# Performance work log

Measured on AMD Instinct MI355X. Metric: run time of the kernel, lower is better.

The kernel has to match this reference:

```python
import jax, jax.numpy as jnp
import numpy as np

N, E = 50000, 800000
D, H, EDIM, DFF = 128, 8, 16, 512
C = D // H  # per-head channels
NEG_SLOPE_GAT = 0.2
NEG_SLOPE = 0.01
EPS_LN = 1e-6


def layer_norm(x, g, b):
    mu = x.mean(-1, keepdims=True)
    sd = x.std(-1, keepdims=True, ddof=1)  # torch std default (unbiased)
    return g * (x - mu) / (sd + EPS_LN) + b


def gat_conv(x, ei, ew, W, a_src, a_dst, We, a_e, bias):
    # PyG GATConv with edge_dim, concat=True, eval mode (no dropout)
    n = x.shape[0]
    xh = (x @ W).reshape(n, H, C)            # [N,H,C]
    s_src = (xh * a_src).sum(-1)             # [N,H]
    s_dst = (xh * a_dst).sum(-1)             # [N,H]
    eh = (ew @ We).reshape(-1, H, C)         # [E,H,C]
    s_e = (eh * a_e).sum(-1)                 # [E,H]
    src, dst = ei[0], ei[1]
    alpha = jax.nn.leaky_relu(s_src[src] + s_dst[dst] + s_e, NEG_SLOPE_GAT)  # [E,H]
    # segment softmax over destination nodes
    m = jax.ops.segment_max(alpha, dst, num_segments=n)
    alpha = jnp.exp(alpha - m[dst])
    z = jax.ops.segment_sum(alpha, dst, num_segments=n)
    alpha = alpha / (z[dst] + 1e-16)
    msg = xh[src] * alpha[..., None]         # [E,H,C]
    out = jax.ops.segment_sum(msg, dst, num_segments=n)  # [N,H,C]
    return out.reshape(n, H * C) + bias


def setup_inputs() -> dict:
    key = jax.random.key(0)
    ks = jax.random.split(key, 32)
    p = lambda k, sh: (jax.random.normal(k, sh, dtype=jnp.float32) * 0.02)
    inp = {
        "nf": jax.random.normal(ks[0], (N, D), dtype=jnp.float32),
        "ei": jax.random.randint(ks[1], (2, E), 0, N, dtype=jnp.int32),
        "ew": jax.random.normal(ks[2], (E, EDIM), dtype=jnp.float32),
        # GATConv 1
        "W1": p(ks[3], (D, H * C)), "as1": p(ks[4], (H, C)), "ad1": p(ks[5], (H, C)),
        "We1": p(ks[6], (EDIM, H * C)), "ae1": p(ks[7], (H, C)), "b1": jnp.zeros((H * C,), jnp.float32),
        "g1": jnp.ones((D,), jnp.float32), "be1": jnp.zeros((D,), jnp.float32),
        # GATConv 2
        "W2": p(ks[8], (D, H * C)), "as2": p(ks[9], (H, C)), "ad2": p(ks[10], (H, C)),
        "We2": p(ks[11], (EDIM, H * C)), "ae2": p(ks[12], (H, C)), "b2": jnp.zeros((H * C,), jnp.float32),
        "g2": jnp.ones((D,), jnp.float32), "be2": jnp.zeros((D,), jnp.float32),
        # FFN + norm3
        "Wf1": p(ks[13], (D, DFF)), "bf1": jnp.zeros((DFF,), jnp.float32),
        "Wf2": p(ks[14], (DFF, D)), "bf2": jnp.zeros((D,), jnp.float32),
        "g3": jnp.ones((D,), jnp.float32), "be3": jnp.zeros((D,), jnp.float32),
    }
    return inp


def reference(nf, ei, ew, W1, as1, ad1, We1, ae1, b1, g1, be1,
              W2, as2, ad2, We2, ae2, b2, g2, be2,
              Wf1, bf1, Wf2, bf2, g3, be3):
    # gnn_mode == 'res', eval mode (dropout = identity)
    h = gat_conv(nf, ei, ew, W1, as1, ad1, We1, ae1, b1)
    nf = nf + jax.nn.leaky_relu(layer_norm(h, g1, be1), NEG_SLOPE)
    h = gat_conv(nf, ei, ew, W2, as2, ad2, We2, ae2, b2)
    nf = nf + jax.nn.leaky_relu(layer_norm(h, g2, be2), NEG_SLOPE)
    ff = jax.nn.relu(nf @ Wf1 + bf1) @ Wf2 + bf2
    nf = nf + jax.nn.leaky_relu(layer_norm(ff, g3, be3), NEG_SLOPE)
    return nf
```

## Files before the change

kernel.cpp:

```cpp
#include <hip/hip_runtime.h>
#include <hip/hip_bf16.h>

#define NN 50000
#define NE 800000
#define DD 128
#define HH 8
#define CC 16
#define DFF 512
#define ED 16
#define SCAN_NB ((NN + 255) / 256)
#define BKT 256
#define NBKT ((NN + BKT - 1) / BKT)
#define EPB 4096

typedef __attribute__((ext_vector_type(8))) short bf16x8;
typedef __attribute__((ext_vector_type(4))) float f32x4;

union U8 { bf16x8 v; unsigned short s[8]; };

__device__ inline unsigned short f2bf(float f) {
    union { float f; unsigned u; } v; v.f = f;
    return (unsigned short)((v.u + 0x7fffu + ((v.u >> 16) & 1u)) >> 16);
}
__device__ inline float bf2f(unsigned s) {
    union { unsigned u; float f; } v; v.u = s << 16;
    return v.f;
}

__global__ void zero_int_k(int* __restrict__ a, int n) {
    int i = blockIdx.x * 256 + threadIdx.x;
    if (i < n) a[i] = 0;
}

__global__ void cvtpack_k(const float* __restrict__ W, unsigned short* __restrict__ Wpk,
                          int K, int N) {
    int idx = blockIdx.x * 256 + threadIdx.x;
    if (idx >= K * N) return;
    int e = idx & 7;
    int l = (idx >> 3) & 63;
    int r = idx >> 9;
    int n16 = N >> 4;
    int jc = r % n16;
    int kt = r / n16;
    int k = kt * 32 + (l >> 4) * 8 + e;
    int n = jc * 16 + (l & 15);
    Wpk[idx] = f2bf(W[(size_t)k * N + n]);
}

__global__ void count_k(const int* __restrict__ dst, int* __restrict__ cnt) {
    int e = blockIdx.x * 256 + threadIdx.x;
    if (e < NE) atomicAdd(&cnt[dst[e]], 1);
}

__global__ void blksum_k(const int* __restrict__ cnt, int* __restrict__ partials) {
    int i = blockIdx.x * 256 + threadIdx.x;
    int v = (i < NN) ? cnt[i] : 0;
#pragma unroll
    for (int m = 1; m < 64; m <<= 1) v += __shfl_xor(v, m, 64);
    __shared__ int ws[4];
    if ((threadIdx.x & 63) == 0) ws[threadIdx.x >> 6] = v;
    __syncthreads();
    if (threadIdx.x == 0) partials[blockIdx.x] = ws[0] + ws[1] + ws[2] + ws[3];
}

__global__ void scanpart_k(int* __restrict__ partials) {
    __shared__ int buf[256];
    int t = threadIdx.x;
    int v = (t < SCAN_NB) ? partials[t] : 0;
    buf[t] = v;
    __syncthreads();
    for (int off = 1; off < 256; off <<= 1) {
        int u = (t >= off) ? buf[t - off] : 0;
        __syncthreads();
        buf[t] += u;
        __syncthreads();
    }
    if (t < SCAN_NB) partials[t] = buf[t] - v;
}

__global__ void scanapply_k(const int* __restrict__ cnt, const int* __restrict__ partials,
                            int* __restrict__ row_start, int* __restrict__ cursor) {
    __shared__ int buf[256];
    int t = threadIdx.x;
    int i = blockIdx.x * 256 + t;
    int v = (i < NN) ? cnt[i] : 0;
    buf[t] = v;
    __syncthreads();
    for (int off = 1; off < 256; off <<= 1) {
        int u = (t >= off) ? buf[t - off] : 0;
        __syncthreads();
        buf[t] += u;
        __syncthreads();
    }
    int excl = buf[t] - v + partials[blockIdx.x];
    if (i < NN) {
        row_start[i] = excl;
        cursor[i] = excl;
        if (i == NN - 1) row_start[NN] = excl + v;
    }
}

__global__ void bucketbase_k(const int* __restrict__ row_start, int* __restrict__ bucket_cursor) {
    int b = blockIdx.x * 256 + threadIdx.x;
    if (b < NBKT) bucket_cursor[b] = row_start[b * BKT];
}

__global__ __launch_bounds__(256) void bin_k(const int* __restrict__ ei,
                                             int* __restrict__ bucket_cursor,
                                             int2* __restrict__ binned) {
    __shared__ int hist[NBKT];
    __shared__ int base[NBKT];
    int t = threadIdx.x;
    int e0 = blockIdx.x * EPB;
    int eend = e0 + EPB; if (eend > NE) eend = NE;
    if (t < NBKT) hist[t] = 0;
    __syncthreads();
    for (int e = e0 + t; e < eend; e += 256) {
        int d = ei[NE + e];
        atomicAdd(&hist[d >> 8], 1);
    }
    __syncthreads();
    if (t < NBKT) {
        int c = hist[t];
        base[t] = c ? atomicAdd(&bucket_cursor[t], c) : 0;
        hist[t] = 0;
    }
    __syncthreads();
    for (int e = e0 + t; e < eend; e += 256) {
        int s = ei[e];
        int d = ei[NE + e];
        int b = d >> 8;
        int loc = atomicAdd(&hist[b], 1);
        binned[base[b] + loc] = make_int2(s | ((d & 255) << 16), e);
    }
}

__global__ __launch_bounds__(256) void csr_scatter_k(const int2* __restrict__ binned,
                                                     const int* __restrict__ row_start,
                                                     int* __restrict__ cursor,
                                                     int* __restrict__ e_src,
                                                     int* __restrict__ e_eid) {
    int b = blockIdx.x;
    int beg = row_start[b * BKT];
    int endNode = (b + 1) * BKT; if (endNode > NN) endNode = NN;
    int end = row_start[endNode];
    for (int p = beg + threadIdx.x; p < end; p += 256) {
        int2 r = binned[p];
        int d = b * BKT + (r.x >> 16);
        int pos = atomicAdd(&cursor[d], 1);
        e_src[pos] = r.x & 0xffff;
        e_eid[pos] = r.y;
    }
}

__global__ void se2_k(const float* __restrict__ ew, const int* __restrict__ e_eid,
                      const float* __restrict__ We1, const float* __restrict__ ae1,
                      const float* __restrict__ We2, const float* __restrict__ ae2,
                      float* __restrict__ s_e1, float* __restrict__ s_e2) {
    __shared__ float A1[ED * HH], A2[ED * HH];
    int t = threadIdx.x;
    if (t < 128) {
        int k = t >> 3, h = t & 7;
        float s = 0.f;
#pragma unroll
        for (int c = 0; c < CC; c++) s += We1[k * DD + h * CC + c] * ae1[h * CC + c];
        A1[t] = s;
    } else {
        int u = t - 128;
        int k = u >> 3, h = u & 7;
        float s = 0.f;
#pragma unroll
        for (int c = 0; c < CC; c++) s += We2[k * DD + h * CC + c] * ae2[h * CC + c];
        A2[u] = s;
    }
    __syncthreads();
    int p = blockIdx.x * 256 + t;
    if (p >= NE) return;
    int eid = e_eid[p];
    const float* ep = &ew[(size_t)eid * ED];
    float4 v0 = *(const float4*)(ep);
    float4 v1 = *(const float4*)(ep + 4);
    float4 v2 = *(const float4*)(ep + 8);
    float4 v3 = *(const float4*)(ep + 12);
    float ev[16] = {v0.x, v0.y, v0.z, v0.w, v1.x, v1.y, v1.z, v1.w,
                    v2.x, v2.y, v2.z, v2.w, v3.x, v3.y, v3.z, v3.w};
    float o1[8] = {0, 0, 0, 0, 0, 0, 0, 0};
    float o2[8] = {0, 0, 0, 0, 0, 0, 0, 0};
#pragma unroll
    for (int k = 0; k < 16; k++) {
        float v = ev[k];
#pragma unroll
        for (int h = 0; h < 8; h++) {
            o1[h] += v * A1[k * 8 + h];
            o2[h] += v * A2[k * 8 + h];
        }
    }
    *(float4*)&s_e1[(size_t)p * 8]     = make_float4(o1[0], o1[1], o1[2], o1[3]);
    *(float4*)&s_e1[(size_t)p * 8 + 4] = make_float4(o1[4], o1[5], o1[6], o1[7]);
    *(float4*)&s_e2[(size_t)p * 8]     = make_float4(o2[0], o2[1], o2[2], o2[3]);
    *(float4*)&s_e2[(size_t)p * 8 + 4] = make_float4(o2[4], o2[5], o2[6], o2[7]);
}

__global__ __launch_bounds__(256) void gemm_mfma_k(const float* __restrict__ X,
                                                   const unsigned short* __restrict__ Wpk,
                                                   unsigned short* __restrict__ Ybf) {
    __shared__ char Xl[128 * 256];
    int t = threadIdx.x;
    int nb0 = blockIdx.x * 128;
    for (int c = t; c < 2048; c += 256) {
        int row = c >> 4, cb = c & 15;
        int n = nb0 + row;
        U8 u;
        if (n < NN) {
            const float* xp = &X[(size_t)n * DD + cb * 8];
            float4 a = *(const float4*)xp;
            float4 b = *(const float4*)(xp + 4);
            u.s[0] = f2bf(a.x); u.s[1] = f2bf(a.y); u.s[2] = f2bf(a.z); u.s[3] = f2bf(a.w);
            u.s[4] = f2bf(b.x); u.s[5] = f2bf(b.y); u.s[6] = f2bf(b.z); u.s[7] = f2bf(b.w);
        } else {
#pragma unroll
            for (int q = 0; q < 8; q++) u.s[q] = 0;
        }
        int byte = (row * 256 + cb * 16) ^ ((row & 7) << 4);
        *(bf16x8*)&Xl[byte] = u.v;
    }
    __syncthreads();
    int w = t >> 6, l = t & 63;
    int lrow = l & 15, lq = l >> 4;
    int r0 = (w & 1) * 64, c0 = (w >> 1) * 64;
    f32x4 acc[4][4];
#pragma unroll
    for (int i = 0; i < 4; i++)
#pragma unroll
        for (int j = 0; j < 4; j++) acc[i][j] = (f32x4){0.f, 0.f, 0.f, 0.f};
#pragma unroll
    for (int ks = 0; ks < 4; ks++) {
        int k0 = ks * 32;
        bf16x8 af[4], bq[4];
#pragma unroll
        for (int i = 0; i < 4; i++) {
            int rr = r0 + i * 16 + lrow;
            int byte = (rr * 256 + k0 * 2 + lq * 16) ^ ((rr & 7) << 4);
            af[i] = *(const bf16x8*)&Xl[byte];
        }
#pragma unroll
        for (int j = 0; j < 4; j++) {
            int j16 = (c0 >> 4) + j;
            bq[j] = *(const bf16x8*)&Wpk[(((size_t)ks * 8 + j16) * 64 + l) * 8];
        }
#pragma unroll
        for (int i = 0; i < 4; i++)
#pragma unroll
            for (int j = 0; j < 4; j++)
                acc[i][j] = __builtin_amdgcn_mfma_f32_16x16x32_bf16(af[i], bq[j], acc[i][j], 0, 0, 0);
    }
#pragma unroll
    for (int i = 0; i < 4; i++) {
#pragma unroll
        for (int j = 0; j < 4; j++) {
#pragma unroll
            for (int q = 0; q < 4; q++) {
                int n = nb0 + r0 + i * 16 + lq * 4 + q;
                if (n < NN) Ybf[(size_t)n * DD + c0 + j * 16 + lrow] = f2bf(acc[i][j][q]);
            }
        }
    }
}

__global__ void ssd_k(const unsigned short* __restrict__ xh_bf, const float* __restrict__ a_src,
                      const float* __restrict__ a_dst, float* __restrict__ s_src,
                      float* __restrict__ s_dst) {
    __shared__ float as[128], ad[128];
    if (threadIdx.x < 128) {
        as[threadIdx.x] = a_src[threadIdx.x];
        ad[threadIdx.x] = a_dst[threadIdx.x];
    }
    __syncthreads();
    int idx = blockIdx.x * 256 + threadIdx.x;
    if (idx >= NN * HH) return;
    int n = idx >> 3, h = idx & 7;
    const unsigned short* x = &xh_bf[(size_t)n * DD + h * CC];
    U8 u0, u1;
    u0.v = *(const bf16x8*)(x);
    u1.v = *(const bf16x8*)(x + 8);
    float s1 = 0.f, s2 = 0.f;
#pragma unroll
    for (int c = 0; c < 8; c++) {
        float v = bf2f(u0.s[c]);
        s1 += v * as[h * CC + c];
        s2 += v * ad[h * CC + c];
    }
#pragma unroll
    for (int c = 0; c < 8; c++) {
        float v = bf2f(u1.s[c]);
        s1 += v * as[h * CC + 8 + c];
        s2 += v * ad[h * CC + 8 + c];
    }
    s_src[idx] = s1;
    s_dst[idx] = s2;
}

__global__ __launch_bounds__(256) void agg_ln_k(const int* __restrict__ row_start,
                                                const int* __restrict__ e_src,
                                                const float* __restrict__ s_src,
                                                const float* __restrict__ s_dst,
                                                const float* __restrict__ s_e,
                                                const unsigned short* __restrict__ xh_bf,
                                                const float* __restrict__ bias,
                                                const float* __restrict__ g,
                                                const float* __restrict__ be,
                                                const float* __restrict__ res,
                                                float* __restrict__ outNf) {
    int wid = (blockIdx.x * 256 + threadIdx.x) >> 6;
    if (wid >= NN) return;
    int lane = threadIdx.x & 63;
    int h = lane >> 3;
    int k = lane & 7;
    unsigned hoff = (unsigned)h << 2;
    unsigned loff = (unsigned)lane << 2;
    const char* xb = (const char*)xh_bf;
    const char* sb = (const char*)s_src;
    const char* eb = (const char*)s_e;
    float sdst = s_dst[wid * 8 + h];
    int beg = row_start[wid], end = row_start[wid + 1];
    float acc0 = 0.f, acc1 = 0.f, zpart = 0.f, ztail = 0.f;
    int p = beg;
    int bcast = h << 3;
    for (; p + 8 <= end; p += 8) {
        unsigned q = (unsigned)e_src[p + k];
        float vs = *(const float*)(sb + (q << 5) + hoff);
        float ve = *(const float*)(eb + (((unsigned)(p + k)) << 5) + hoff);
        float a = vs + sdst + ve;
        a = fmaxf(a, 0.2f * a);
        float esc = __expf(a);
        zpart += esc;
#pragma unroll
        for (int kk = 0; kk < 8; kk++) {
            float sck = __shfl(esc, bcast + kk, 64);
            unsigned qk = (unsigned)__shfl((int)q, kk, 64);
            unsigned u = *(const unsigned*)(xb + (qk << 8) + loff);
            acc0 = fmaf(sck, bf2f(u & 0xffffu), acc0);
            acc1 = fmaf(sck, bf2f(u >> 16), acc1);
        }
    }
    for (; p < end; p++) {
        unsigned q0 = (unsigned)e_src[p];
        float a0 = *(const float*)(sb + (q0 << 5) + hoff) + sdst + *(const float*)(eb + ((unsigned)p << 5) + hoff);
        unsigned u0 = *(const unsigned*)(xb + (q0 << 8) + loff);
        a0 = fmaxf(a0, 0.2f * a0);
        float e0 = __expf(a0);
        ztail += e0;
        acc0 = fmaf(e0, bf2f(u0 & 0xffffu), acc0);
        acc1 = fmaf(e0, bf2f(u0 >> 16), acc1);
    }
    float z = zpart;
    z += __shfl_xor(z, 1, 64);
    z += __shfl_xor(z, 2, 64);
    z += __shfl_xor(z, 4, 64);
    z += ztail;
    float inv = 1.f / (z + 1e-16f);
    float2 b = *(const float2*)&bias[lane * 2];
    float x0 = acc0 * inv + b.x;
    float x1 = acc1 * inv + b.y;
    float s = x0 + x1;
    float q = x0 * x0 + x1 * x1;
#pragma unroll
    for (int m = 1; m < 64; m <<= 1) {
        s += __shfl_xor(s, m, 64);
        q += __shfl_xor(q, m, 64);
    }
    float mu = s * (1.f / 128.f);
    float var = (q - 128.f * mu * mu) * (1.f / 127.f);
    float sd = sqrtf(fmaxf(var, 0.f));
    float invs = 1.f / (sd + 1e-6f);
    float2 gg = *(const float2*)&g[lane * 2];
    float2 bb = *(const float2*)&be[lane * 2];
    float y0 = gg.x * (x0 - mu) * invs + bb.x;
    float y1 = gg.y * (x1 - mu) * invs + bb.y;
    y0 = (y0 > 0.f) ? y0 : 0.01f * y0;
    y1 = (y1 > 0.f) ? y1 : 0.01f * y1;
    float2 r = *(const float2*)&res[(size_t)wid * DD + lane * 2];
    *(float2*)&outNf[(size_t)wid * DD + lane * 2] = make_float2(r.x + y0, r.y + y1);
}

__global__ __launch_bounds__(256) void ln_k(const float* __restrict__ hin,
                                            const float* __restrict__ bias,
                                            const float* __restrict__ g,
                                            const float* __restrict__ be,
                                            const float* __restrict__ res,
                                            float* __restrict__ out) {
    int wid = (blockIdx.x * 256 + threadIdx.x) >> 6;
    if (wid >= NN) return;
    int lane = threadIdx.x & 63;
    float2 x = *(const float2*)&hin[(size_t)wid * DD + lane * 2];
    float2 b = *(const float2*)&bias[lane * 2];
    x.x += b.x;
    x.y += b.y;
    float s = x.x + x.y;
    float q = x.x * x.x + x.y * x.y;
#pragma unroll
    for (int m = 1; m < 64; m <<= 1) {
        s += __shfl_xor(s, m, 64);
        q += __shfl_xor(q, m, 64);
    }
    float mu = s * (1.f / 128.f);
    float var = (q - 128.f * mu * mu) * (1.f / 127.f);
    float sd = sqrtf(fmaxf(var, 0.f));
    float inv = 1.f / (sd + 1e-6f);
    float2 gg = *(const float2*)&g[lane * 2];
    float2 bb = *(const float2*)&be[lane * 2];
    float y0 = gg.x * (x.x - mu) * inv + bb.x;
    float y1 = gg.y * (x.y - mu) * inv + bb.y;
    y0 = (y0 > 0.f) ? y0 : 0.01f * y0;
    y1 = (y1 > 0.f) ? y1 : 0.01f * y1;
    float2 r = *(const float2*)&res[(size_t)wid * DD + lane * 2];
    *(float2*)&out[(size_t)wid * DD + lane * 2] = make_float2(r.x + y0, r.y + y1);
}

__global__ __launch_bounds__(256) void ffn_mfma_k(const float* __restrict__ X,
                                                  const unsigned short* __restrict__ Wf1pk,
                                                  const float* __restrict__ bf1,
                                                  const unsigned short* __restrict__ Wf2pk,
                                                  float* __restrict__ out) {
    __shared__ char Xl[64 * 256];
    __shared__ char Hl[64 * 256];
    int t = threadIdx.x;
    int nb0 = blockIdx.x * 64;
    for (int c = t; c < 1024; c += 256) {
        int row = c >> 4, cb = c & 15;
        int n = nb0 + row;
        U8 u;
        if (n < NN) {
            const float* xp = &X[(size_t)n * DD + cb * 8];
            float4 a = *(const float4*)xp;
            float4 b = *(const float4*)(xp + 4);
            u.s[0] = f2bf(a.x); u.s[1] = f2bf(a.y); u.s[2] = f2bf(a.z); u.s[3] = f2bf(a.w);
            u.s[4] = f2bf(b.x); u.s[5] = f2bf(b.y); u.s[6] = f2bf(b.z); u.s[7] = f2bf(b.w);
        } else {
#pragma unroll
            for (int q = 0; q < 8; q++) u.s[q] = 0;
        }
        int byte = (row * 256 + cb * 16) ^ ((row & 7) << 4);
        *(bf16x8*)&Xl[byte] = u.v;
    }
    __syncthreads();
    int w = t >> 6, l = t & 63;
    int lrow = l & 15, lq = l >> 4;
    int wr = (w & 1) * 32;
    int wc = (w >> 1) * 64;
    f32x4 oacc[2][4];
#pragma unroll
    for (int i = 0; i < 2; i++)
#pragma unroll
        for (int j = 0; j < 4; j++) oacc[i][j] = (f32x4){0.f, 0.f, 0.f, 0.f};

#pragma unroll
    for (int ch = 0; ch < 4; ch++) {
        int hc0 = ch * 128;
        f32x4 a[2][4];
#pragma unroll
        for (int i = 0; i < 2; i++)
#pragma unroll
            for (int j = 0; j < 4; j++) a[i][j] = (f32x4){0.f, 0.f, 0.f, 0.f};
#pragma unroll
        for (int ks = 0; ks < 4; ks++) {
            int k0 = ks * 32;
            bf16x8 af[2], bq[4];
#pragma unroll
            for (int i = 0; i < 2; i++) {
                int rr = wr + i * 16 + lrow;
                int byte = (rr * 256 + k0 * 2 + lq * 16) ^ ((rr & 7) << 4);
                af[i] = *(const bf16x8*)&Xl[byte];
            }
#pragma unroll
            for (int j = 0; j < 4; j++) {
                int j16 = ch * 8 + (wc >> 4) + j;
                bq[j] = *(const bf16x8*)&Wf1pk[(((size_t)ks * 32 + j16) * 64 + l) * 8];
            }
#pragma unroll
            for (int i = 0; i < 2; i++)
#pragma unroll
                for (int j = 0; j < 4; j++)
                    a[i][j] = __builtin_amdgcn_mfma_f32_16x16x32_bf16(af[i], bq[j], a[i][j], 0, 0, 0);
        }
        float bias[4];
#pragma unroll
        for (int j = 0; j < 4; j++) bias[j] = bf1[hc0 + wc + j * 16 + lrow];
#pragma unroll
        for (int i = 0; i < 2; i++) {
#pragma unroll
            for (int j = 0; j < 4; j++) {
#pragma unroll
                for (int q = 0; q < 4; q++) {
                    float v = fmaxf(a[i][j][q] + bias[j], 0.f);
                    int row = wr + i * 16 + lq * 4 + q;
                    int col = wc + j * 16 + lrow;
                    int byte = (row * 256 + col * 2) ^ ((row & 7) << 4);
                    *(unsigned short*)&Hl[byte] = f2bf(v);
                }
            }
        }
        __syncthreads();
#pragma unroll
        for (int ks = 0; ks < 4; ks++) {
            int k0 = ks * 32;
            bf16x8 hf[2], b2[4];
#pragma unroll
            for (int i = 0; i < 2; i++) {
                int rr = wr + i * 16 + lrow;
                int byte = (rr * 256 + k0 * 2 + lq * 16) ^ ((rr & 7) << 4);
                hf[i] = *(const bf16x8*)&Hl[byte];
            }
#pragma unroll
            for (int j = 0; j < 4; j++) {
                int kt = ch * 4 + ks;
                int j16 = (wc >> 4) + j;
                b2[j] = *(const bf16x8*)&Wf2pk[(((size_t)kt * 8 + j16) * 64 + l) * 8];
            }
#pragma unroll
            for (int i = 0; i < 2; i++)
#pragma unroll
                for (int j = 0; j < 4; j++)
                    oacc[i][j] = __builtin_amdgcn_mfma_f32_16x16x32_bf16(hf[i], b2[j], oacc[i][j], 0, 0, 0);
        }
        __syncthreads();
    }
#pragma unroll
    for (int i = 0; i < 2; i++) {
#pragma unroll
        for (int j = 0; j < 4; j++) {
#pragma unroll
            for (int q = 0; q < 4; q++) {
                int n = nb0 + wr + i * 16 + lq * 4 + q;
                if (n < NN) out[(size_t)n * DD + wc + j * 16 + lrow] = oacc[i][j][q];
            }
        }
    }
}

extern "C" void kernel_launch(void* const* d_in, const int* in_sizes, int n_in,
                              void* d_out, int out_size, void* d_ws, size_t ws_size,
                              hipStream_t stream) {
    const float* nf  = (const float*)d_in[0];
    const int*   ei  = (const int*)d_in[1];
    const float* ew  = (const float*)d_in[2];
    const float* W1  = (const float*)d_in[3];
    const float* as1 = (const float*)d_in[4];
    const float* ad1 = (const float*)d_in[5];
    const float* We1 = (const float*)d_in[6];
    const float* ae1 = (const float*)d_in[7];
    const float* b1  = (const float*)d_in[8];
    const float* g1  = (const float*)d_in[9];
    const float* be1 = (const float*)d_in[10];
    const float* W2  = (const float*)d_in[11];
    const float* as2 = (const float*)d_in[12];
    const float* ad2 = (const float*)d_in[13];
    const float* We2 = (const float*)d_in[14];
    const float* ae2 = (const float*)d_in[15];
    const float* b2  = (const float*)d_in[16];
    const float* g2  = (const float*)d_in[17];
    const float* be2 = (const float*)d_in[18];
    const float* Wf1 = (const float*)d_in[19];
    const float* bf1 = (const float*)d_in[20];
    const float* Wf2 = (const float*)d_in[21];
    const float* bf2 = (const float*)d_in[22];
    const float* g3  = (const float*)d_in[23];
    const float* be3 = (const float*)d_in[24];
    float* out = (float*)d_out;

    char* p = (char*)d_ws;
    auto alloc = [&](size_t bytes) {
        char* r = p;
        p += (bytes + 255) & ~(size_t)255;
        return r;
    };
    float* nf_cur = (float*)alloc((size_t)NN * DD * 4);
    unsigned short* xh_bf = (unsigned short*)alloc((size_t)NN * DD * 2);
    float* s_e1   = (float*)alloc((size_t)NE * HH * 4);
    float* s_e2   = (float*)alloc((size_t)NE * HH * 4);
    float* s_src  = (float*)alloc((size_t)NN * HH * 4);
    float* s_dst  = (float*)alloc((size_t)NN * HH * 4);
    int* row_start = (int*)alloc((size_t)(NN + 1) * 4);
    int* cnt       = (int*)alloc((size_t)NN * 4);
    int* cursor    = (int*)alloc((size_t)NN * 4);
    int* partials  = (int*)alloc((size_t)SCAN_NB * 4);
    int* bucket_cursor = (int*)alloc((size_t)NBKT * 4);
    int2* binned   = (int2*)alloc((size_t)NE * 8);
    int* e_src     = (int*)alloc((size_t)NE * 4);
    int* e_eid     = (int*)alloc((size_t)NE * 4);
    unsigned short* W1pk  = (unsigned short*)alloc((size_t)DD * DD * 2);
    unsigned short* W2pk  = (unsigned short*)alloc((size_t)DD * DD * 2);
    unsigned short* Wf1pk = (unsigned short*)alloc((size_t)DD * DFF * 2);
    unsigned short* Wf2pk = (unsigned short*)alloc((size_t)DFF * DD * 2);
    float* h_out = s_e1;

    int ebl = (NE + 255) / 256;
    int nbl = (NN + 255) / 256;

    cvtpack_k<<<(DD * DD + 255) / 256, 256, 0, stream>>>(W1, W1pk, DD, DD);
    cvtpack_k<<<(DD * DD + 255) / 256, 256, 0, stream>>>(W2, W2pk, DD, DD);
    cvtpack_k<<<(DD * DFF + 255) / 256, 256, 0, stream>>>(Wf1, Wf1pk, DD, DFF);
    cvtpack_k<<<(DD * DFF + 255) / 256, 256, 0, stream>>>(Wf2, Wf2pk, DFF, DD);

    zero_int_k<<<nbl, 256, 0, stream>>>(cnt, NN);
    count_k<<<ebl, 256, 0, stream>>>(ei + NE, cnt);
    blksum_k<<<SCAN_NB, 256, 0, stream>>>(cnt, partials);
    scanpart_k<<<1, 256, 0, stream>>>(partials);
    scanapply_k<<<SCAN_NB, 256, 0, stream>>>(cnt, partials, row_start, cursor);

    bucketbase_k<<<(NBKT + 255) / 256, 256, 0, stream>>>(row_start, bucket_cursor);
    bin_k<<<(NE + EPB - 1) / EPB, 256, 0, stream>>>(ei, bucket_cursor, binned);
    csr_scatter_k<<<NBKT, 256, 0, stream>>>(binned, row_start, cursor, e_src, e_eid);

    se2_k<<<ebl, 256, 0, stream>>>(ew, e_eid, We1, ae1, We2, ae2, s_e1, s_e2);

    int gbl = (NN + 127) / 128;
    int wbl = (NN + 3) / 4;
    int sbl = (NN * HH + 255) / 256;

    gemm_mfma_k<<<gbl, 256, 0, stream>>>(nf, W1pk, xh_bf);
    ssd_k<<<sbl, 256, 0, stream>>>(xh_bf, as1, ad1, s_src, s_dst);
    agg_ln_k<<<wbl, 256, 0, stream>>>(row_start, e_src, s_src, s_dst, s_e1, xh_bf,
                                      b1, g1, be1, nf, nf_cur);

    gemm_mfma_k<<<gbl, 256, 0, stream>>>(nf_cur, W2pk, xh_bf);
    ssd_k<<<sbl, 256, 0, stream>>>(xh_bf, as2, ad2, s_src, s_dst);
    agg_ln_k<<<wbl, 256, 0, stream>>>(row_start, e_src, s_src, s_dst, s_e2, xh_bf,
                                      b2, g2, be2, nf_cur, nf_cur);

    ffn_mfma_k<<<(NN + 63) / 64, 256, 0, stream>>>(nf_cur, Wf1pk, bf1, Wf2pk, h_out);
    ln_k<<<wbl, 256, 0, stream>>>(h_out, bf2, g3, be3, nf_cur, out);
}
```

Baseline: 302.9 us.

## Store attention logits in bf16 and fuse final LayerNorm into FFN kernel

Edge and source attention scores (s_e1, s_e2, s_src) are now stored as bf16 instead of fp32, halving their footprint and the gather traffic in the aggregation kernel. The FFN kernel now stages its output tile in shared memory and applies bias, LayerNorm, leaky ReLU and the residual in place. This removes the separate ln_k launch and the global round trip of the FFN output. The cost is reduced precision on the softmax logits, plus extra LDS traffic and a barrier at the end of the FFN kernel.

```diff
diff --git a/kernel.cpp b/kernel.cpp
--- a/kernel.cpp
+++ b/kernel.cpp
@@ -156,7 +156,7 @@
 __global__ void se2_k(const float* __restrict__ ew, const int* __restrict__ e_eid,
                       const float* __restrict__ We1, const float* __restrict__ ae1,
                       const float* __restrict__ We2, const float* __restrict__ ae2,
-                      float* __restrict__ s_e1, float* __restrict__ s_e2) {
+                      unsigned short* __restrict__ s_e1, unsigned short* __restrict__ s_e2) {
     __shared__ float A1[ED * HH], A2[ED * HH];
     int t = threadIdx.x;
     if (t < 128) {
@@ -195,10 +195,11 @@
             o2[h] += v * A2[k * 8 + h];
         }
     }
-    *(float4*)&s_e1[(size_t)p * 8]     = make_float4(o1[0], o1[1], o1[2], o1[3]);
-    *(float4*)&s_e1[(size_t)p * 8 + 4] = make_float4(o1[4], o1[5], o1[6], o1[7]);
-    *(float4*)&s_e2[(size_t)p * 8]     = make_float4(o2[0], o2[1], o2[2], o2[3]);
-    *(float4*)&s_e2[(size_t)p * 8 + 4] = make_float4(o2[4], o2[5], o2[6], o2[7]);
+    U8 w1, w2;
+#pragma unroll
+    for (int h = 0; h < 8; h++) { w1.s[h] = f2bf(o1[h]); w2.s[h] = f2bf(o2[h]); }
+    *(bf16x8*)&s_e1[(size_t)p * 8] = w1.v;
+    *(bf16x8*)&s_e2[(size_t)p * 8] = w2.v;
 }
 
 __global__ __launch_bounds__(256) void gemm_mfma_k(const float* __restrict__ X,
@@ -268,7 +269,7 @@
 }
 
 __global__ void ssd_k(const unsigned short* __restrict__ xh_bf, const float* __restrict__ a_src,
-                      const float* __restrict__ a_dst, float* __restrict__ s_src,
+                      const float* __restrict__ a_dst, unsigned short* __restrict__ s_srcb,
                       float* __restrict__ s_dst) {
     __shared__ float as[128], ad[128];
     if (threadIdx.x < 128) {
@@ -296,15 +297,15 @@
         s1 += v * as[h * CC + 8 + c];
         s2 += v * ad[h * CC + 8 + c];
     }
-    s_src[idx] = s1;
+    s_srcb[idx] = f2bf(s1);
     s_dst[idx] = s2;
 }
 
 __global__ __launch_bounds__(256) void agg_ln_k(const int* __restrict__ row_start,
                                                 const int* __restrict__ e_src,
-                                                const float* __restrict__ s_src,
+                                                const unsigned short* __restrict__ s_srcb,
                                                 const float* __restrict__ s_dst,
-                                                const float* __restrict__ s_e,
+                                                const unsigned short* __restrict__ s_eb,
                                                 const unsigned short* __restrict__ xh_bf,
                                                 const float* __restrict__ bias,
                                                 const float* __restrict__ g,
@@ -316,11 +317,11 @@
     int lane = threadIdx.x & 63;
     int h = lane >> 3;
     int k = lane & 7;
-    unsigned hoff = (unsigned)h << 2;
+    unsigned h2 = (unsigned)h << 1;
     unsigned loff = (unsigned)lane << 2;
     const char* xb = (const char*)xh_bf;
-    const char* sb = (const char*)s_src;
-    const char* eb = (const char*)s_e;
+    const char* sb = (const char*)s_srcb;
+    const char* eb = (const char*)s_eb;
     float sdst = s_dst[wid * 8 + h];
     int beg = row_start[wid], end = row_start[wid + 1];
     float acc0 = 0.f, acc1 = 0.f, zpart = 0.f, ztail = 0.f;
@@ -328,8 +329,8 @@
     int bcast = h << 3;
     for (; p + 8 <= end; p += 8) {
         unsigned q = (unsigned)e_src[p + k];
-        float vs = *(const float*)(sb + (q << 5) + hoff);
-        float ve = *(const float*)(eb + (((unsigned)(p + k)) << 5) + hoff);
+        float vs = bf2f(*(const unsigned short*)(sb + (q << 4) + h2));
+        float ve = bf2f(*(const unsigned short*)(eb + (((unsigned)(p + k)) << 4) + h2));
         float a = vs + sdst + ve;
         a = fmaxf(a, 0.2f * a);
         float esc = __expf(a);
@@ -345,7 +346,8 @@
     }
     for (; p < end; p++) {
         unsigned q0 = (unsigned)e_src[p];
-        float a0 = *(const float*)(sb + (q0 << 5) + hoff) + sdst + *(const float*)(eb + ((unsigned)p << 5) + hoff);
+        float a0 = bf2f(*(const unsigned short*)(sb + (q0 << 4) + h2)) + sdst
+                 + bf2f(*(const unsigned short*)(eb + ((unsigned)p << 4) + h2));
         unsigned u0 = *(const unsigned*)(xb + (q0 << 8) + loff);
         a0 = fmaxf(a0, 0.2f * a0);
         float e0 = __expf(a0);
@@ -383,47 +385,17 @@
     *(float2*)&outNf[(size_t)wid * DD + lane * 2] = make_float2(r.x + y0, r.y + y1);
 }
 
-__global__ __launch_bounds__(256) void ln_k(const float* __restrict__ hin,
-                                            const float* __restrict__ bias,
-                                            const float* __restrict__ g,
-                                            const float* __restrict__ be,
-                                            const float* __restrict__ res,
-                                            float* __restrict__ out) {
-    int wid = (blockIdx.x * 256 + threadIdx.x) >> 6;
-    if (wid >= NN) return;
-    int lane = threadIdx.x & 63;
-    float2 x = *(const float2*)&hin[(size_t)wid * DD + lane * 2];
-    float2 b = *(const float2*)&bias[lane * 2];
-    x.x += b.x;
-    x.y += b.y;
-    float s = x.x + x.y;
-    float q = x.x * x.x + x.y * x.y;
-#pragma unroll
-    for (int m = 1; m < 64; m <<= 1) {
-        s += __shfl_xor(s, m, 64);
-        q += __shfl_xor(q, m, 64);
-    }
-    float mu = s * (1.f / 128.f);
-    float var = (q - 128.f * mu * mu) * (1.f / 127.f);
-    float sd = sqrtf(fmaxf(var, 0.f));
-    float inv = 1.f / (sd + 1e-6f);
-    float2 gg = *(const float2*)&g[lane * 2];
-    float2 bb = *(const float2*)&be[lane * 2];
-    float y0 = gg.x * (x.x - mu) * inv + bb.x;
-    float y1 = gg.y * (x.y - mu) * inv + bb.y;
-    y0 = (y0 > 0.f) ? y0 : 0.01f * y0;
-    y1 = (y1 > 0.f) ? y1 : 0.01f * y1;
-    float2 r = *(const float2*)&res[(size_t)wid * DD + lane * 2];
-    *(float2*)&out[(size_t)wid * DD + lane * 2] = make_float2(r.x + y0, r.y + y1);
-}
-
-__global__ __launch_bounds__(256) void ffn_mfma_k(const float* __restrict__ X,
-                                                  const unsigned short* __restrict__ Wf1pk,
-                                                  const float* __restrict__ bf1,
-                                                  const unsigned short* __restrict__ Wf2pk,
-                                                  float* __restrict__ out) {
-    __shared__ char Xl[64 * 256];
-    __shared__ char Hl[64 * 256];
+__global__ __launch_bounds__(256) void ffn_ln_k(const float* __restrict__ X,
+                                                const unsigned short* __restrict__ Wf1pk,
+                                                const float* __restrict__ bf1,
+                                                const unsigned short* __restrict__ Wf2pk,
+                                                const float* __restrict__ bf2,
+                                                const float* __restrict__ g3,
+                                                const float* __restrict__ be3,
+                                                float* __restrict__ out) {
+    __shared__ char LDSBUF[32768];
+    char* Xl = LDSBUF;
+    char* Hl = LDSBUF + 16384;
     int t = threadIdx.x;
     int nb0 = blockIdx.x * 64;
     for (int c = t; c < 1024; c += 256) {
@@ -525,16 +497,45 @@
         }
         __syncthreads();
     }
+    float* Ol = (float*)LDSBUF;
 #pragma unroll
     for (int i = 0; i < 2; i++) {
 #pragma unroll
         for (int j = 0; j < 4; j++) {
 #pragma unroll
             for (int q = 0; q < 4; q++) {
-                int n = nb0 + wr + i * 16 + lq * 4 + q;
-                if (n < NN) out[(size_t)n * DD + wc + j * 16 + lrow] = oacc[i][j][q];
+                int row = wr + i * 16 + lq * 4 + q;
+                int col = wc + j * 16 + lrow;
+                Ol[row * 128 + col] = oacc[i][j][q];
             }
         }
+    }
+    __syncthreads();
+    float2 b = *(const float2*)&bf2[l * 2];
+    float2 gg = *(const float2*)&g3[l * 2];
+    float2 bb = *(const float2*)&be3[l * 2];
+    for (int rr = w * 16; rr < w * 16 + 16; rr++) {
+        int n = nb0 + rr;
+        if (n >= NN) continue;
+        float x0 = Ol[rr * 128 + l * 2]     + b.x;
+        float x1 = Ol[rr * 128 + l * 2 + 1] + b.y;
+        float s = x0 + x1;
+        float q = x0 * x0 + x1 * x1;
+#pragma unroll
+        for (int m = 1; m < 64; m <<= 1) {
+            s += __shfl_xor(s, m, 64);
+            q += __shfl_xor(q, m, 64);
+        }
+        float mu = s * (1.f / 128.f);
+        float var = (q - 128.f * mu * mu) * (1.f / 127.f);
+        float sd = sqrtf(fmaxf(var, 0.f));
+        float inv = 1.f / (sd + 1e-6f);
+        float y0 = gg.x * (x0 - mu) * inv + bb.x;
+        float y1 = gg.y * (x1 - mu) * inv + bb.y;
+        y0 = (y0 > 0.f) ? y0 : 0.01f * y0;
+        y1 = (y1 > 0.f) ? y1 : 0.01f * y1;
+        float2 r = *(const float2*)&X[(size_t)n * DD + l * 2];
+        *(float2*)&out[(size_t)n * DD + l * 2] = make_float2(r.x + y0, r.y + y1);
     }
 }
 
@@ -576,9 +577,9 @@
     };
     float* nf_cur = (float*)alloc((size_t)NN * DD * 4);
     unsigned short* xh_bf = (unsigned short*)alloc((size_t)NN * DD * 2);
-    float* s_e1   = (float*)alloc((size_t)NE * HH * 4);
-    float* s_e2   = (float*)alloc((size_t)NE * HH * 4);
-    float* s_src  = (float*)alloc((size_t)NN * HH * 4);
+    unsigned short* s_e1  = (unsigned short*)alloc((size_t)NE * HH * 2);
+    unsigned short* s_e2  = (unsigned short*)alloc((size_t)NE * HH * 2);
+    unsigned short* s_srcb = (unsigned short*)alloc((size_t)NN * HH * 2);
     float* s_dst  = (float*)alloc((size_t)NN * HH * 4);
     int* row_start = (int*)alloc((size_t)(NN + 1) * 4);
     int* cnt       = (int*)alloc((size_t)NN * 4);
@@ -592,7 +593,6 @@
     unsigned short* W2pk  = (unsigned short*)alloc((size_t)DD * DD * 2);
     unsigned short* Wf1pk = (unsigned short*)alloc((size_t)DD * DFF * 2);
     unsigned short* Wf2pk = (unsigned short*)alloc((size_t)DFF * DD * 2);
-    float* h_out = s_e1;
 
     int ebl = (NE + 255) / 256;
     int nbl = (NN + 255) / 256;
@@ -619,15 +619,15 @@
     int sbl = (NN * HH + 255) / 256;
 
     gemm_mfma_k<<<gbl, 256, 0, stream>>>(nf, W1pk, xh_bf);
-    ssd_k<<<sbl, 256, 0, stream>>>(xh_bf, as1, ad1, s_src, s_dst);
-    agg_ln_k<<<wbl, 256, 0, stream>>>(row_start, e_src, s_src, s_dst, s_e1, xh_bf,
+    ssd_k<<<sbl, 256, 0, stream>>>(xh_bf, as1, ad1, s_srcb, s_dst);
+    agg_ln_k<<<wbl, 256, 0, stream>>>(row_start, e_src, s_srcb, s_dst, s_e1, xh_bf,
                                       b1, g1, be1, nf, nf_cur);
 
     gemm_mfma_k<<<gbl, 256, 0, stream>>>(nf_cur, W2pk, xh_bf);
-    ssd_k<<<sbl, 256, 0, stream>>>(xh_bf, as2, ad2, s_src, s_dst);
-    agg_ln_k<<<wbl, 256, 0, stream>>>(row_start, e_src, s_src, s_dst, s_e2, xh_bf,
+    ssd_k<<<sbl, 256, 0, stream>>>(xh_bf, as2, ad2, s_srcb, s_dst);
+    agg_ln_k<<<wbl, 256, 0, stream>>>(row_start, e_src, s_srcb, s_dst, s_e2, xh_bf,
                                       b2, g2, be2, nf_cur, nf_cur);
 
-    ffn_mfma_k<<<(NN + 63) / 64, 256, 0, stream>>>(nf_cur, Wf1pk, bf1, Wf2pk, h_out);
-    ln_k<<<wbl, 256, 0, stream>>>(h_out, bf2, g3, be3, nf_cur, out);
-}
+    ffn_ln_k<<<(NN + 63) / 64, 256, 0, stream>>>(nf_cur, Wf1pk, bf1, Wf2pk,
+                                                 bf2, g3, be3, out);
+}
```

Result: faster. 295.4 us (-2.5%).
